# Optimization experiments

Measured on AMD Instinct MI355X. Metric: run time of the kernel, lower is better.

## Reference

```python
import jax, jax.numpy as jnp
import numpy as np

N_NODES = 100000
N_EDGES = 1600000
N_GRAPHS = 1024
EMB = 32
HID = 64
N_CLASSES = 10
N_SHAPE = 16
N_COLOR = 8


def setup_inputs() -> dict:
    key = jax.random.key(0)
    ks = jax.random.split(key, 12)
    shape_id = jax.random.randint(ks[0], (N_NODES,), 0, N_SHAPE + 1, dtype=jnp.int32)
    color_id = jax.random.randint(ks[1], (N_NODES,), 0, N_COLOR + 1, dtype=jnp.int32)
    edge_index = jax.random.randint(ks[2], (2, N_EDGES), 0, N_NODES, dtype=jnp.int32)
    batch = jnp.sort(jax.random.randint(ks[3], (N_NODES,), 0, N_GRAPHS, dtype=jnp.int32))
    shape_table = jax.random.normal(ks[4], (N_SHAPE + 1, EMB), jnp.float32)
    color_table = jax.random.normal(ks[5], (N_COLOR + 1, EMB), jnp.float32)
    W1 = jax.random.normal(ks[6], (EMB, HID), jnp.float32) / np.sqrt(EMB)
    b1 = jnp.zeros((HID,), jnp.float32)
    W2 = jax.random.normal(ks[7], (HID, HID), jnp.float32) / np.sqrt(HID)
    b2 = jnp.zeros((HID,), jnp.float32)
    Wl = jax.random.normal(ks[8], (HID, N_CLASSES), jnp.float32) / np.sqrt(HID)
    bl = jnp.zeros((N_CLASSES,), jnp.float32)
    return dict(shape_id=shape_id, color_id=color_id, edge_index=edge_index, batch=batch,
                shape_table=shape_table, color_table=color_table,
                W1=W1, b1=b1, W2=W2, b2=b2, Wl=Wl, bl=bl)


def gcn_conv(x, W, b, src, dst, num_nodes):
    # PyG GCNConv: add self-loops, symmetric normalization D^-1/2 (A+I) D^-1/2
    h = x @ W  # [N, out]
    deg = 1.0 + jax.ops.segment_sum(jnp.ones_like(dst, jnp.float32), dst, num_segments=num_nodes)
    dis = jax.lax.rsqrt(deg)  # deg >= 1 due to self-loop
    norm = dis[src] * dis[dst]  # [E]
    agg = jax.ops.segment_sum(h[src] * norm[:, None], dst, num_segments=num_nodes)
    agg = agg + h * (dis * dis)[:, None]  # self-loop term
    return agg + b


def reference(shape_id, color_id, edge_index, batch, shape_table, color_table,
              W1, b1, W2, b2, Wl, bl):
    # padding_idx=0 -> row 0 contributes zeros
    st = shape_table.at[0].set(0.0)
    ct = color_table.at[0].set(0.0)
    x = st[shape_id] + ct[color_id]  # [N, emb]
    src, dst = edge_index[0], edge_index[1]
    x = jax.nn.relu(gcn_conv(x, W1, b1, src, dst, N_NODES))
    x = jax.nn.relu(gcn_conv(x, W2, b2, src, dst, N_NODES))
    # global_mean_pool over batch ids
    sums = jax.ops.segment_sum(x, batch, num_segments=N_GRAPHS)
    cnts = jax.ops.segment_sum(jnp.ones((x.shape[0],), x.dtype), batch, num_segments=N_GRAPHS)
    pooled = sums / jnp.maximum(cnts, 1.0)[:, None]  # [B, hidden]
    return pooled @ Wl + bl  # [B, num_classes]
```

## Files before the change

### kernel.cpp

```cpp
#include <hip/hip_runtime.h>
#include <hip/hip_bf16.h>
#include <hip/hip_fp16.h>

#define N_NODES   100000
#define N_EDGES   1600000
#define N_GRAPHS  1024
#define EMB       32
#define HID       64
#define N_CLASSES 10
#define SCAN_BLOCKS 391
#define NCOMBO 153
#define BUCK_NODES 448
#define NBUCK 224
#define BIN_CAP 8192
#define EPB 4096

typedef _Float16 f16x8 __attribute__((ext_vector_type(8)));
typedef float f32x4 __attribute__((ext_vector_type(4)));

__global__ __launch_bounds__(256) void prep_kernel(
    const int* __restrict__ sid, const int* __restrict__ cid,
    const int* __restrict__ batch, int* __restrict__ combo, int* __restrict__ gstart,
    const float* __restrict__ st, const float* __restrict__ ct,
    const float* __restrict__ W1, __half* __restrict__ TCh,
    float* __restrict__ pooled, int* __restrict__ gcur) {
    int t = threadIdx.x;
    int v = blockIdx.x * 256 + t;
    if (v < N_GRAPHS * HID) pooled[v] = 0.0f;
    if (blockIdx.x == 0 && t < NBUCK) gcur[t] = 0;
    if (v < N_NODES) {
        combo[v] = sid[v] * 9 + cid[v];
        int b = batch[v];
        int bp = (v == 0) ? -1 : batch[v - 1];
        for (int g = bp + 1; g <= b; ++g) gstart[g] = v;
        if (v == N_NODES - 1) {
            for (int g = b + 1; g <= N_GRAPHS; ++g) gstart[g] = N_NODES;
        }
    }
    if (blockIdx.x < NCOMBO && t >= 64 && t < 128) {
        int r = blockIdx.x, j = t - 64;
        int s = r / 9, c = r % 9;
        float acc = 0.0f;
        if (s != 0) {
#pragma unroll
            for (int k = 0; k < EMB; ++k) acc = fmaf(st[s * EMB + k], W1[k * HID + j], acc);
        }
        if (c != 0) {
#pragma unroll
            for (int k = 0; k < EMB; ++k) acc = fmaf(ct[c * EMB + k], W1[k * HID + j], acc);
        }
        TCh[r * HID + j] = __float2half_rn(acc);
    }
}

__global__ __launch_bounds__(512) void binA_kernel(
    const int* __restrict__ src, const int* __restrict__ dst,
    int* __restrict__ gcur, int* __restrict__ gbin) {
    __shared__ int2 stg[EPB];
    __shared__ int hist[NBUCK];
    __shared__ int base[NBUCK + 1];
    __shared__ int gstart[NBUCK];
    __shared__ int scanbuf[256];
    int t = threadIdx.x;
    int e0 = blockIdx.x * EPB;
    for (int i = t; i < NBUCK; i += 512) hist[i] = 0;
    __syncthreads();

    int2 myq[8];
    int mybo[8];
    if (e0 + EPB <= N_EDGES) {
        int eb = e0 + t * 8;
        int4 sa4 = *(const int4*)&src[eb];
        int4 sb4 = *(const int4*)&src[eb + 4];
        int4 da4 = *(const int4*)&dst[eb];
        int4 db4 = *(const int4*)&dst[eb + 4];
        int ss[8] = {sa4.x, sa4.y, sa4.z, sa4.w, sb4.x, sb4.y, sb4.z, sb4.w};
        int dd[8] = {da4.x, da4.y, da4.z, da4.w, db4.x, db4.y, db4.z, db4.w};
#pragma unroll
        for (int i = 0; i < 8; ++i) {
            unsigned b = (unsigned)dd[i] / BUCK_NODES;
            int off = atomicAdd(&hist[b], 1);
            myq[i].x = ss[i];
            myq[i].y = dd[i];
            mybo[i] = (int)(b << 16) | off;
        }
    } else {
#pragma unroll
        for (int i = 0; i < 8; ++i) {
            int e = e0 + t * 8 + i;
            if (e < N_EDGES) {
                int d = dst[e];
                unsigned b = (unsigned)d / BUCK_NODES;
                int off = atomicAdd(&hist[b], 1);
                myq[i].x = src[e];
                myq[i].y = d;
                mybo[i] = (int)(b << 16) | off;
            } else {
                mybo[i] = -1;
            }
        }
    }
    __syncthreads();

    int h = (t < NBUCK) ? hist[t] : 0;
    if (t < 256) scanbuf[t] = h;
    __syncthreads();
#pragma unroll
    for (int off = 1; off < 256; off <<= 1) {
        int x = (t < 256 && t >= off) ? scanbuf[t - off] : 0;
        __syncthreads();
        if (t < 256) scanbuf[t] += x;
        __syncthreads();
    }
    if (t < NBUCK) base[t] = scanbuf[t] - h;
    if (t == 0) base[NBUCK] = scanbuf[255];
    __syncthreads();
#pragma unroll
    for (int i = 0; i < 8; ++i) {
        if (mybo[i] >= 0) {
            int b = mybo[i] >> 16, off = mybo[i] & 0xFFFF;
            stg[base[b] + off] = myq[i];
        }
    }
    if (t < NBUCK) {
        int n = hist[t];
        gstart[t] = n ? atomicAdd(&gcur[t], n) : 0;
    }
    __syncthreads();
    int total = base[NBUCK];
    for (int i = t; i < total; i += 512) {
        int2 q = stg[i];
        unsigned b = (unsigned)q.y / BUCK_NODES;
        int local = q.y - (int)b * BUCK_NODES;
        gbin[(size_t)b * BIN_CAP + gstart[b] + (i - base[b])] = q.x | (local << 17);
    }
}

__global__ __launch_bounds__(1024) void bucket_scatter_kernel(
    const int* __restrict__ gbin, const int* __restrict__ gcur,
    float* __restrict__ dis, int* __restrict__ rowptr, int* __restrict__ epack4) {
    __shared__ __align__(16) int pbin[BIN_CAP];
    __shared__ int ldeg[BUCK_NODES];
    __shared__ int rbase[BUCK_NODES];
    __shared__ int s[512];
    __shared__ int sc[256];
    int b = blockIdx.x, t = threadIdx.x;
    if (t < 256) sc[t] = (t < NBUCK) ? gcur[t] : 0;
    for (int i = t; i < BUCK_NODES; i += 1024) ldeg[i] = 0;
    __syncthreads();
#pragma unroll
    for (int off = 1; off < 256; off <<= 1) {
        int x = (t < 256 && t >= off) ? sc[t - off] : 0;
        __syncthreads();
        if (t < 256) sc[t] += x;
        __syncthreads();
    }
    int bb = (b == 0) ? 0 : sc[b - 1];
    int n = gcur[b];
    int nc = (n + 3) >> 2;
    {
        const int4* my4 = (const int4*)(gbin + (size_t)b * BIN_CAP);
        for (int c = t; c < nc; c += 1024) {
            int4 p4 = my4[c];
            ((int4*)pbin)[c] = p4;
            int i0 = c * 4;
            if (i0 + 0 < n) atomicAdd(&ldeg[(unsigned)p4.x >> 17], 1);
            if (i0 + 1 < n) atomicAdd(&ldeg[(unsigned)p4.y >> 17], 1);
            if (i0 + 2 < n) atomicAdd(&ldeg[(unsigned)p4.z >> 17], 1);
            if (i0 + 3 < n) atomicAdd(&ldeg[(unsigned)p4.w >> 17], 1);
        }
    }
    __syncthreads();
    int d = (t < BUCK_NODES) ? ldeg[t] : 0;
    int v = b * BUCK_NODES + t;
    if (t < BUCK_NODES && v < N_NODES) dis[v] = rsqrtf(1.0f + (float)d);
    if (t < 512) s[t] = d;
    __syncthreads();
#pragma unroll
    for (int off = 1; off < 512; off <<= 1) {
        int x = (t < 512 && t >= off) ? s[t - off] : 0;
        __syncthreads();
        if (t < 512) s[t] += x;
        __syncthreads();
    }
    if (t < BUCK_NODES) {
        int rp = bb + s[t] - d;
        rbase[t] = rp;
        if (v < N_NODES) rowptr[v] = rp;
    }
    if (b == 0 && t == 0) rowptr[N_NODES] = N_EDGES;
    for (int i = t; i < BUCK_NODES; i += 1024) ldeg[i] = 0;
    __syncthreads();
    for (int i = t; i < n; i += 1024) {
        int p = pbin[i];
        int local = (unsigned)p >> 17;
        int r = atomicAdd(&ldeg[local], 1);
        epack4[rbase[local] + r] = p & 0x1FFFF;
    }
}

#define AGG_CHUNK(CQ, DQ, LBASE, J0)                                           \
    _Pragma("unroll")                                                          \
    for (int i = 0; i < 8; ++i) {                                              \
        int off = __builtin_amdgcn_readlane((CQ), (LBASE) + i) & 0x7FFF;       \
        int wb  = __builtin_amdgcn_readlane(__float_as_int(DQ), (LBASE) + i);  \
        off = ((J0) + i < cnt) ? off : 0;                                      \
        wb  = ((J0) + i < cnt) ? wb  : 0;                                      \
        __half tv = *(const __half*)((const char*)TCs + (off + lane2));        \
        acc = fmaf(__int_as_float(wb), __half2float(tv), acc);                 \
    }

#define AGG_NODE(N, RS, RE, DV, CO)                                            \
    {                                                                          \
        int deg = (RE) - (RS);                                                 \
        int cnt = deg > 32 ? 32 : deg;                                         \
        float acc = 0.0f;                                                      \
        AGG_CHUNK(cq1, dq1, (N)*16, 0)                                         \
        if (cnt > 8)  { AGG_CHUNK(cq1, dq1, (N)*16 + 8, 8) }                   \
        if (cnt > 16) { AGG_CHUNK(cq2, dq2, (N)*16, 16) }                      \
        if (cnt > 24) { AGG_CHUNK(cq2, dq2, (N)*16 + 8, 24) }                  \
        if (deg > 32) {                                                        \
            for (int e = (RS) + 32; e < (RE); ++e) {                           \
                int qx = epack4[e];                                            \
                float dw = dis[qx];                                            \
                __half tv = *(const __half*)((const char*)TCs +                \
                                             ((combo[qx] << 7) + lane2));      \
                acc = fmaf(dw, __half2float(tv), acc);                         \
            }                                                                  \
        }                                                                      \
        __half hv = *(const __half*)((const char*)TCs + ((CO) + lane2));       \
        float val = (DV) * fmaf(__half2float(hv), (DV), acc) + bias;           \
        val = val > 0.0f ? val : 0.0f;                                         \
        xsA[w * 4 + (N)][lane] = __float2half_rn(val * (DV));                  \
    }

__global__ __launch_bounds__(256, 6) void agg1_mm2_kernel(
    const int* __restrict__ epack4, const int* __restrict__ rowptr,
    const int* __restrict__ combo, const float* __restrict__ dis,
    const __half* __restrict__ TCh, const float* __restrict__ W2,
    const float* __restrict__ b1, __half* __restrict__ h2s) {
    __shared__ __align__(16) __half TCs[NCOMBO * HID];
    __shared__ __align__(16) __half xsA[16][72];
    __shared__ __align__(16) __half Dst[16 * 64];
    int t = threadIdx.x;
    int lane = t & 63, w = t >> 6;
    int lane2 = lane * 2;
    int vb = blockIdx.x * 16;
    int v0 = vb + w * 4;

    int sub = lane >> 4, sl = lane & 15;
    int rb = rowptr[v0 + sub];
    int q1x = epack4[rb + sl] & 0x1FFFF;
    int q2x = epack4[rb + 16 + sl] & 0x1FFFF;
    float dq1 = dis[q1x];
    float dq2 = dis[q2x];
    int cq1 = combo[q1x] << 7;
    int cq2 = combo[q2x] << 7;

    int r0 = __builtin_amdgcn_readfirstlane(rowptr[v0]);
    int r1 = __builtin_amdgcn_readfirstlane(rowptr[v0 + 1]);
    int r2 = __builtin_amdgcn_readfirstlane(rowptr[v0 + 2]);
    int r3 = __builtin_amdgcn_readfirstlane(rowptr[v0 + 3]);
    int r4 = __builtin_amdgcn_readfirstlane(rowptr[v0 + 4]);

    float d0 = dis[v0], d1 = dis[v0 + 1], d2 = dis[v0 + 2], d3 = dis[v0 + 3];
    int o0 = combo[v0] << 7, o1 = combo[v0 + 1] << 7;
    int o2 = combo[v0 + 2] << 7, o3 = combo[v0 + 3] << 7;
    float bias = b1[lane];

    f16x8 bf0, bf1;
    {
        int colw = (w << 4) + (lane & 15);
        int kb = (lane >> 4) * 8;
#pragma unroll
        for (int i = 0; i < 8; ++i) {
            bf0[i] = (_Float16)W2[(kb + i) * HID + colw];
            bf1[i] = (_Float16)W2[(32 + kb + i) * HID + colw];
        }
    }

    {
        const int4* s4 = (const int4*)TCh;
        int4* dd4 = (int4*)TCs;
        for (int i = t; i < NCOMBO * HID * 2 / 16; i += 256) dd4[i] = s4[i];
    }
    __syncthreads();

    AGG_NODE(0, r0, r1, d0, o0)
    AGG_NODE(1, r1, r2, d1, o1)
    AGG_NODE(2, r2, r3, d2, o2)
    AGG_NODE(3, r3, r4, d3, o3)

    __syncthreads();

    const __half* xa = &xsA[lane & 15][0];
    f16x8 a0 = *(const f16x8*)(xa + (lane >> 4) * 8);
    f16x8 a1 = *(const f16x8*)(xa + 32 + (lane >> 4) * 8);
    f32x4 dacc = {0.0f, 0.0f, 0.0f, 0.0f};
    dacc = __builtin_amdgcn_mfma_f32_16x16x32_f16(a0, bf0, dacc, 0, 0, 0);
    dacc = __builtin_amdgcn_mfma_f32_16x16x32_f16(a1, bf1, dacc, 0, 0, 0);

    {
        int colg = (w << 4) + (lane & 15);
#pragma unroll
        for (int i = 0; i < 4; ++i)
            Dst[((lane >> 4) * 4 + i) * 64 + colg] = __float2half_rn(dacc[i]);
    }
    __syncthreads();

    {
        const uint2* ds2 = (const uint2*)Dst;
        uint2* go = (uint2*)(h2s + (size_t)vb * HID);
        go[t] = ds2[t];
    }
}

__device__ __forceinline__ float agg2_node(const int* __restrict__ epack4, int sx,
                                           int rs, int re, int lane, int lane2,
                                           const __half* __restrict__ h2s) {
    float acc = 0.0f;
    int p = rs;
    for (;;) {
        int avail = re - p;
        int cnt = avail > 64 ? 64 : avail;
        int vo = sx << 7;
        int j = 0;
        for (; j + 8 <= cnt; j += 8) {
            float g[8];
#pragma unroll
            for (int i = 0; i < 8; ++i) {
                int off = __builtin_amdgcn_readlane(vo, j + i);
                g[i] = __half2float(*(const __half*)((const char*)h2s + (off + lane2)));
            }
#pragma unroll
            for (int i = 0; i < 8; ++i) acc += g[i];
        }
        if (j < cnt) {
#pragma unroll
            for (int i = 0; i < 8; ++i) {
                int jj = j + i;
                int off = __builtin_amdgcn_readlane(vo, jj & 63);
                float gv = __half2float(*(const __half*)((const char*)h2s + (off + lane2)));
                acc += (jj < cnt) ? gv : 0.0f;
            }
        }
        p += 64;
        if (p >= re) break;
        int idx = p + lane;
        idx = idx < N_EDGES ? idx : N_EDGES - 1;
        sx = epack4[idx];
    }
    return acc;
}

__global__ __launch_bounds__(256, 8) void agg2_pool_kernel(
    const int* __restrict__ epack4, const int* __restrict__ rowptr,
    const __half* __restrict__ h2s, const float* __restrict__ dis,
    const float* __restrict__ b2, const int* __restrict__ batch,
    float* __restrict__ pooled) {
    int t = threadIdx.x, lane = t & 63, w = t >> 6;
    int lane2 = lane * 2;
    int v0 = (blockIdx.x * 4 + w) * 4;

    int r0 = __builtin_amdgcn_readfirstlane(rowptr[v0]);
    int r1 = __builtin_amdgcn_readfirstlane(rowptr[v0 + 1]);
    int r2 = __builtin_amdgcn_readfirstlane(rowptr[v0 + 2]);
    int r3 = __builtin_amdgcn_readfirstlane(rowptr[v0 + 3]);
    int r4 = __builtin_amdgcn_readfirstlane(rowptr[v0 + 4]);

    int ia = r0 + lane; ia = ia < N_EDGES ? ia : N_EDGES - 1;
    int ib = r1 + lane; ib = ib < N_EDGES ? ib : N_EDGES - 1;
    int ic = r2 + lane; ic = ic < N_EDGES ? ic : N_EDGES - 1;
    int id = r3 + lane; id = id < N_EDGES ? id : N_EDGES - 1;
    int sa = epack4[ia];
    int sb = epack4[ib];
    int sc = epack4[ic];
    int sd = epack4[id];

    float bv = b2[lane];
    float acc0 = agg2_node(epack4, sa, r0, r1, lane, lane2, h2s);
    float acc1 = agg2_node(epack4, sb, r1, r2, lane, lane2, h2s);
    float acc2 = agg2_node(epack4, sc, r2, r3, lane, lane2, h2s);
    float acc3 = agg2_node(epack4, sd, r3, r4, lane, lane2, h2s);

#define AGG2_VAL(V, ACC, OUT)                                                  \
    {                                                                          \
        float dv = dis[V];                                                     \
        float self = __half2float(h2s[(size_t)(V) * HID + lane]);              \
        float val = dv * ((ACC) + self) + bv;                                  \
        OUT = val > 0.0f ? val : 0.0f;                                         \
    }
    float val0, val1, val2, val3;
    AGG2_VAL(v0, acc0, val0)
    AGG2_VAL(v0 + 1, acc1, val1)
    AGG2_VAL(v0 + 2, acc2, val2)
    AGG2_VAL(v0 + 3, acc3, val3)
#undef AGG2_VAL

    int g0 = __builtin_amdgcn_readfirstlane(batch[v0]);
    int g1 = __builtin_amdgcn_readfirstlane(batch[v0 + 1]);
    int g2 = __builtin_amdgcn_readfirstlane(batch[v0 + 2]);
    int g3 = __builtin_amdgcn_readfirstlane(batch[v0 + 3]);
    float s = val0; int g = g0;
    if (g1 == g) { s += val1; } else { unsafeAtomicAdd(&pooled[g * HID + lane], s); g = g1; s = val1; }
    if (g2 == g) { s += val2; } else { unsafeAtomicAdd(&pooled[g * HID + lane], s); g = g2; s = val2; }
    if (g3 == g) { s += val3; } else { unsafeAtomicAdd(&pooled[g * HID + lane], s); g = g3; s = val3; }
    unsafeAtomicAdd(&pooled[g * HID + lane], s);
}

__global__ __launch_bounds__(64) void logits_kernel(
    const float* __restrict__ pooled, const int* __restrict__ gstart,
    const float* __restrict__ Wl, const float* __restrict__ bl,
    float* __restrict__ out) {
    __shared__ float row[HID];
    int g = blockIdx.x, t = threadIdx.x;
    int c = gstart[g + 1] - gstart[g]; if (c < 1) c = 1;
    row[t] = pooled[g * HID + t] / (float)c;
    __syncthreads();
    if (t < N_CLASSES) {
        float acc = bl[t];
#pragma unroll
        for (int k = 0; k < HID; ++k) acc = fmaf(row[k], Wl[k * N_CLASSES + t], acc);
        out[g * N_CLASSES + t] = acc;
    }
}

extern "C" void kernel_launch(void* const* d_in, const int* in_sizes, int n_in,
                              void* d_out, int out_size, void* d_ws, size_t ws_size,
                              hipStream_t stream) {
    const int*   shape_id = (const int*)d_in[0];
    const int*   color_id = (const int*)d_in[1];
    const int*   edge_idx = (const int*)d_in[2];
    const int*   batch    = (const int*)d_in[3];
    const float* st       = (const float*)d_in[4];
    const float* ct       = (const float*)d_in[5];
    const float* W1       = (const float*)d_in[6];
    const float* b1       = (const float*)d_in[7];
    const float* W2       = (const float*)d_in[8];
    const float* b2       = (const float*)d_in[9];
    const float* Wl       = (const float*)d_in[10];
    const float* bl       = (const float*)d_in[11];
    float* out = (float*)d_out;

    const int* src = edge_idx;
    const int* dst = edge_idx + N_EDGES;

    char* ws = (char*)d_ws;
    int*    combo   = (int*)   (ws + 0);
    float*  dis     = (float*) (ws + 400384);
    int*    gstart  = (int*)   (ws + 801792);
    int*    rowptr  = (int*)   (ws + 1201152);
    __half* TCh     = (__half*)(ws + 1603584);
    float*  pooled  = (float*) (ws + 1623552);
    int*    gcur    = (int*)   (ws + 1889792);
    int*    epack4  = (int*)   (ws + 1890816);
    int*    gbin    = (int*)   (ws + 14690816);
    __half* h2s     = (__half*)(ws + 29370880);

    prep_kernel<<<SCAN_BLOCKS, 256, 0, stream>>>(shape_id, color_id, batch, combo, gstart,
                                                 st, ct, W1, TCh, pooled, gcur);

    binA_kernel<<<(N_EDGES + EPB - 1) / EPB, 512, 0, stream>>>(src, dst, gcur, gbin);

    bucket_scatter_kernel<<<NBUCK, 1024, 0, stream>>>(gbin, gcur, dis, rowptr, epack4);

    agg1_mm2_kernel<<<6250, 256, 0, stream>>>(epack4, rowptr, combo, dis, TCh, W2, b1, h2s);

    agg2_pool_kernel<<<6250, 256, 0, stream>>>(epack4, rowptr, h2s, dis, b2, batch, pooled);

    logits_kernel<<<N_GRAPHS, 64, 0, stream>>>(pooled, gstart, Wl, bl, out);
}
```

Before: 185.9 us.

## Pad CSR rows to multiples of eight with sentinel node, drop tail masking

Measured after the change: 179.5 us. -3.4%, faster.

```diff
diff --git a/kernel.cpp b/kernel.cpp
--- a/kernel.cpp
+++ b/kernel.cpp
@@ -14,6 +14,8 @@
 #define NBUCK 224
 #define BIN_CAP 8192
 #define EPB 4096
+#define PBCAP 11328
+#define SENTINEL N_NODES
 
 typedef _Float16 f16x8 __attribute__((ext_vector_type(8)));
 typedef float f32x4 __attribute__((ext_vector_type(4)));
@@ -23,11 +25,15 @@
     const int* __restrict__ batch, int* __restrict__ combo, int* __restrict__ gstart,
     const float* __restrict__ st, const float* __restrict__ ct,
     const float* __restrict__ W1, __half* __restrict__ TCh,
-    float* __restrict__ pooled, int* __restrict__ gcur) {
+    float* __restrict__ pooled, int* __restrict__ gcur, __half* __restrict__ h2s) {
     int t = threadIdx.x;
     int v = blockIdx.x * 256 + t;
     if (v < N_GRAPHS * HID) pooled[v] = 0.0f;
-    if (blockIdx.x == 0 && t < NBUCK) gcur[t] = 0;
+    if (blockIdx.x == 0) {
+        if (t < NBUCK) gcur[t] = 0;
+        if (t == 0) combo[N_NODES] = 0;
+        if (t < 32) ((float*)(h2s + (size_t)N_NODES * HID))[t] = 0.0f;
+    }
     if (v < N_NODES) {
         combo[v] = sid[v] * 9 + cid[v];
         int b = batch[v];
@@ -143,19 +149,9 @@
     __shared__ int ldeg[BUCK_NODES];
     __shared__ int rbase[BUCK_NODES];
     __shared__ int s[512];
-    __shared__ int sc[256];
     int b = blockIdx.x, t = threadIdx.x;
-    if (t < 256) sc[t] = (t < NBUCK) ? gcur[t] : 0;
     for (int i = t; i < BUCK_NODES; i += 1024) ldeg[i] = 0;
     __syncthreads();
-#pragma unroll
-    for (int off = 1; off < 256; off <<= 1) {
-        int x = (t < 256 && t >= off) ? sc[t - off] : 0;
-        __syncthreads();
-        if (t < 256) sc[t] += x;
-        __syncthreads();
-    }
-    int bb = (b == 0) ? 0 : sc[b - 1];
     int n = gcur[b];
     int nc = (n + 3) >> 2;
     {
@@ -174,7 +170,10 @@
     int d = (t < BUCK_NODES) ? ldeg[t] : 0;
     int v = b * BUCK_NODES + t;
     if (t < BUCK_NODES && v < N_NODES) dis[v] = rsqrtf(1.0f + (float)d);
-    if (t < 512) s[t] = d;
+    if (b == 0 && t == 0) dis[N_NODES] = 0.0f;
+    int dp = (d + 7) & ~7;
+    if (dp > 248) dp = 248;
+    if (t < 512) s[t] = dp;
     __syncthreads();
 #pragma unroll
     for (int off = 1; off < 512; off <<= 1) {
@@ -183,45 +182,46 @@
         if (t < 512) s[t] += x;
         __syncthreads();
     }
+    int rp = 0;
+    if (t < 512) rp = b * PBCAP + s[t] - dp;
     if (t < BUCK_NODES) {
-        int rp = bb + s[t] - d;
         rbase[t] = rp;
-        if (v < N_NODES) rowptr[v] = rp;
-    }
-    if (b == 0 && t == 0) rowptr[N_NODES] = N_EDGES;
+        if (v < N_NODES) rowptr[v] = rp | (dp << 24);
+    }
     for (int i = t; i < BUCK_NODES; i += 1024) ldeg[i] = 0;
     __syncthreads();
+    if (t < BUCK_NODES) {
+        for (int k = d; k < dp; ++k) epack4[rp + k] = SENTINEL;
+    }
     for (int i = t; i < n; i += 1024) {
         int p = pbin[i];
         int local = (unsigned)p >> 17;
         int r = atomicAdd(&ldeg[local], 1);
-        epack4[rbase[local] + r] = p & 0x1FFFF;
-    }
-}
-
-#define AGG_CHUNK(CQ, DQ, LBASE, J0)                                           \
+        if (r < 248) epack4[rbase[local] + r] = p & 0x1FFFF;
+    }
+}
+
+#define AGG_CHUNK(CQ, DQ, LBASE)                                               \
     _Pragma("unroll")                                                          \
     for (int i = 0; i < 8; ++i) {                                              \
-        int off = __builtin_amdgcn_readlane((CQ), (LBASE) + i) & 0x7FFF;       \
+        int off = __builtin_amdgcn_readlane((CQ), (LBASE) + i);                \
         int wb  = __builtin_amdgcn_readlane(__float_as_int(DQ), (LBASE) + i);  \
-        off = ((J0) + i < cnt) ? off : 0;                                      \
-        wb  = ((J0) + i < cnt) ? wb  : 0;                                      \
         __half tv = *(const __half*)((const char*)TCs + (off + lane2));        \
         acc = fmaf(__int_as_float(wb), __half2float(tv), acc);                 \
     }
 
-#define AGG_NODE(N, RS, RE, DV, CO)                                            \
+#define AGG_NODE(N, RP, DEG, DV, CO)                                           \
     {                                                                          \
-        int deg = (RE) - (RS);                                                 \
+        int deg = (DEG);                                                       \
         int cnt = deg > 32 ? 32 : deg;                                         \
         float acc = 0.0f;                                                      \
-        AGG_CHUNK(cq1, dq1, (N)*16, 0)                                         \
-        if (cnt > 8)  { AGG_CHUNK(cq1, dq1, (N)*16 + 8, 8) }                   \
-        if (cnt > 16) { AGG_CHUNK(cq2, dq2, (N)*16, 16) }                      \
-        if (cnt > 24) { AGG_CHUNK(cq2, dq2, (N)*16 + 8, 24) }                  \
+        if (cnt > 0)  { AGG_CHUNK(cq1, dq1, (N)*16) }                          \
+        if (cnt > 8)  { AGG_CHUNK(cq1, dq1, (N)*16 + 8) }                      \
+        if (cnt > 16) { AGG_CHUNK(cq2, dq2, (N)*16) }                          \
+        if (cnt > 24) { AGG_CHUNK(cq2, dq2, (N)*16 + 8) }                      \
         if (deg > 32) {                                                        \
-            for (int e = (RS) + 32; e < (RE); ++e) {                           \
-                int qx = epack4[e];                                            \
+            for (int e = (RP) + 32; e < (RP) + deg; ++e) {                     \
+                int qx = epack4[e] & 0x1FFFF;                                  \
                 float dw = dis[qx];                                            \
                 __half tv = *(const __half*)((const char*)TCs +                \
                                              ((combo[qx] << 7) + lane2));      \
@@ -234,14 +234,13 @@
         xsA[w * 4 + (N)][lane] = __float2half_rn(val * (DV));                  \
     }
 
-__global__ __launch_bounds__(256, 6) void agg1_mm2_kernel(
+__global__ __launch_bounds__(256, 8) void agg1_mm2_kernel(
     const int* __restrict__ epack4, const int* __restrict__ rowptr,
     const int* __restrict__ combo, const float* __restrict__ dis,
     const __half* __restrict__ TCh, const float* __restrict__ W2,
     const float* __restrict__ b1, __half* __restrict__ h2s) {
     __shared__ __align__(16) __half TCs[NCOMBO * HID];
     __shared__ __align__(16) __half xsA[16][72];
-    __shared__ __align__(16) __half Dst[16 * 64];
     int t = threadIdx.x;
     int lane = t & 63, w = t >> 6;
     int lane2 = lane * 2;
@@ -249,7 +248,7 @@
     int v0 = vb + w * 4;
 
     int sub = lane >> 4, sl = lane & 15;
-    int rb = rowptr[v0 + sub];
+    int rb = rowptr[v0 + sub] & 0xFFFFFF;
     int q1x = epack4[rb + sl] & 0x1FFFF;
     int q2x = epack4[rb + 16 + sl] & 0x1FFFF;
     float dq1 = dis[q1x];
@@ -257,11 +256,14 @@
     int cq1 = combo[q1x] << 7;
     int cq2 = combo[q2x] << 7;
 
-    int r0 = __builtin_amdgcn_readfirstlane(rowptr[v0]);
-    int r1 = __builtin_amdgcn_readfirstlane(rowptr[v0 + 1]);
-    int r2 = __builtin_amdgcn_readfirstlane(rowptr[v0 + 2]);
-    int r3 = __builtin_amdgcn_readfirstlane(rowptr[v0 + 3]);
-    int r4 = __builtin_amdgcn_readfirstlane(rowptr[v0 + 4]);
+    int r0p = __builtin_amdgcn_readfirstlane(rowptr[v0]);
+    int r1p = __builtin_amdgcn_readfirstlane(rowptr[v0 + 1]);
+    int r2p = __builtin_amdgcn_readfirstlane(rowptr[v0 + 2]);
+    int r3p = __builtin_amdgcn_readfirstlane(rowptr[v0 + 3]);
+    int r0 = r0p & 0xFFFFFF, g0 = (int)((unsigned)r0p >> 24);
+    int r1 = r1p & 0xFFFFFF, g1 = (int)((unsigned)r1p >> 24);
+    int r2 = r2p & 0xFFFFFF, g2 = (int)((unsigned)r2p >> 24);
+    int r3 = r3p & 0xFFFFFF, g3 = (int)((unsigned)r3p >> 24);
 
     float d0 = dis[v0], d1 = dis[v0 + 1], d2 = dis[v0 + 2], d3 = dis[v0 + 3];
     int o0 = combo[v0] << 7, o1 = combo[v0 + 1] << 7;
@@ -286,20 +288,22 @@
     }
     __syncthreads();
 
-    AGG_NODE(0, r0, r1, d0, o0)
-    AGG_NODE(1, r1, r2, d1, o1)
-    AGG_NODE(2, r2, r3, d2, o2)
-    AGG_NODE(3, r3, r4, d3, o3)
+    AGG_NODE(0, r0, g0, d0, o0)
+    AGG_NODE(1, r1, g1, d1, o1)
+    AGG_NODE(2, r2, g2, d2, o2)
+    AGG_NODE(3, r3, g3, d3, o3)
 
     __syncthreads();
 
     const __half* xa = &xsA[lane & 15][0];
     f16x8 a0 = *(const f16x8*)(xa + (lane >> 4) * 8);
     f16x8 a1 = *(const f16x8*)(xa + 32 + (lane >> 4) * 8);
+    __syncthreads();
     f32x4 dacc = {0.0f, 0.0f, 0.0f, 0.0f};
     dacc = __builtin_amdgcn_mfma_f32_16x16x32_f16(a0, bf0, dacc, 0, 0, 0);
     dacc = __builtin_amdgcn_mfma_f32_16x16x32_f16(a1, bf1, dacc, 0, 0, 0);
 
+    __half* Dst = (__half*)xsA;
     {
         int colg = (w << 4) + (lane & 15);
 #pragma unroll
@@ -316,16 +320,16 @@
 }
 
 __device__ __forceinline__ float agg2_node(const int* __restrict__ epack4, int sx,
-                                           int rs, int re, int lane, int lane2,
+                                           int rs, int deg, int lane, int lane2,
                                            const __half* __restrict__ h2s) {
     float acc = 0.0f;
     int p = rs;
+    int re = rs + deg;
     for (;;) {
         int avail = re - p;
         int cnt = avail > 64 ? 64 : avail;
         int vo = sx << 7;
-        int j = 0;
-        for (; j + 8 <= cnt; j += 8) {
+        for (int j = 0; j + 8 <= cnt; j += 8) {
             float g[8];
 #pragma unroll
             for (int i = 0; i < 8; ++i) {
@@ -335,20 +339,9 @@
 #pragma unroll
             for (int i = 0; i < 8; ++i) acc += g[i];
         }
-        if (j < cnt) {
-#pragma unroll
-            for (int i = 0; i < 8; ++i) {
-                int jj = j + i;
-                int off = __builtin_amdgcn_readlane(vo, jj & 63);
-                float gv = __half2float(*(const __half*)((const char*)h2s + (off + lane2)));
-                acc += (jj < cnt) ? gv : 0.0f;
-            }
-        }
         p += 64;
         if (p >= re) break;
-        int idx = p + lane;
-        idx = idx < N_EDGES ? idx : N_EDGES - 1;
-        sx = epack4[idx];
+        sx = epack4[p + lane];
     }
     return acc;
 }
@@ -362,26 +355,25 @@
     int lane2 = lane * 2;
     int v0 = (blockIdx.x * 4 + w) * 4;
 
-    int r0 = __builtin_amdgcn_readfirstlane(rowptr[v0]);
-    int r1 = __builtin_amdgcn_readfirstlane(rowptr[v0 + 1]);
-    int r2 = __builtin_amdgcn_readfirstlane(rowptr[v0 + 2]);
-    int r3 = __builtin_amdgcn_readfirstlane(rowptr[v0 + 3]);
-    int r4 = __builtin_amdgcn_readfirstlane(rowptr[v0 + 4]);
-
-    int ia = r0 + lane; ia = ia < N_EDGES ? ia : N_EDGES - 1;
-    int ib = r1 + lane; ib = ib < N_EDGES ? ib : N_EDGES - 1;
-    int ic = r2 + lane; ic = ic < N_EDGES ? ic : N_EDGES - 1;
-    int id = r3 + lane; id = id < N_EDGES ? id : N_EDGES - 1;
-    int sa = epack4[ia];
-    int sb = epack4[ib];
-    int sc = epack4[ic];
-    int sd = epack4[id];
+    int r0p = __builtin_amdgcn_readfirstlane(rowptr[v0]);
+    int r1p = __builtin_amdgcn_readfirstlane(rowptr[v0 + 1]);
+    int r2p = __builtin_amdgcn_readfirstlane(rowptr[v0 + 2]);
+    int r3p = __builtin_amdgcn_readfirstlane(rowptr[v0 + 3]);
+    int r0 = r0p & 0xFFFFFF, dp0 = (int)((unsigned)r0p >> 24);
+    int r1 = r1p & 0xFFFFFF, dp1 = (int)((unsigned)r1p >> 24);
+    int r2 = r2p & 0xFFFFFF, dp2 = (int)((unsigned)r2p >> 24);
+    int r3 = r3p & 0xFFFFFF, dp3 = (int)((unsigned)r3p >> 24);
+
+    int sa = epack4[r0 + lane];
+    int sb = epack4[r1 + lane];
+    int sc = epack4[r2 + lane];
+    int sd = epack4[r3 + lane];
 
     float bv = b2[lane];
-    float acc0 = agg2_node(epack4, sa, r0, r1, lane, lane2, h2s);
-    float acc1 = agg2_node(epack4, sb, r1, r2, lane, lane2, h2s);
-    float acc2 = agg2_node(epack4, sc, r2, r3, lane, lane2, h2s);
-    float acc3 = agg2_node(epack4, sd, r3, r4, lane, lane2, h2s);
+    float acc0 = agg2_node(epack4, sa, r0, dp0, lane, lane2, h2s);
+    float acc1 = agg2_node(epack4, sb, r1, dp1, lane, lane2, h2s);
+    float acc2 = agg2_node(epack4, sc, r2, dp2, lane, lane2, h2s);
+    float acc3 = agg2_node(epack4, sd, r3, dp3, lane, lane2, h2s);
 
 #define AGG2_VAL(V, ACC, OUT)                                                  \
     {                                                                          \
@@ -458,7 +450,7 @@
     __half* h2s     = (__half*)(ws + 29370880);
 
     prep_kernel<<<SCAN_BLOCKS, 256, 0, stream>>>(shape_id, color_id, batch, combo, gstart,
-                                                 st, ct, W1, TCh, pooled, gcur);
+                                                 st, ct, W1, TCh, pooled, gcur, h2s);
 
     binA_kernel<<<(N_EDGES + EPB - 1) / EPB, 512, 0, stream>>>(src, dst, gcur, gbin);
 
```
